# Kernel tuning notes

Measured on AMD Instinct MI355X. Metric: run time of the kernel, lower is better.

The kernel has to match this reference:

```python
import jax, jax.numpy as jnp
import numpy as np


def setup_inputs() -> dict:
    key = jax.random.key(0)
    k1, k2, k3, k4 = jax.random.split(key, 4)
    B, T, C, H = 32, 2048, 384, 64
    x = jax.random.normal(k1, (B, T, C), dtype=jnp.float32)
    # nn.Linear(C, H, bias=False): weight stored [H, C], applied as x @ W.T.
    # We store the transposed [C, H] form directly.
    s = 1.0 / np.sqrt(C)
    Wk = jax.random.normal(k2, (C, H), dtype=jnp.float32) * s
    Wq = jax.random.normal(k3, (C, H), dtype=jnp.float32) * s
    Wv = jax.random.normal(k4, (C, H), dtype=jnp.float32) * s
    return {"x": x, "Wk": Wk, "Wq": Wq, "Wv": Wv}


def reference(x, Wk, Wq, Wv):
    # x: [B, T, C]; Wk/Wq/Wv: [C, H]
    T = x.shape[1]
    H = Wk.shape[1]
    k = jnp.einsum('btc,ch->bth', x, Wk)
    q = jnp.einsum('btc,ch->bth', x, Wq)
    v = jnp.einsum('btc,ch->bth', x, Wv)
    scale = H ** (-0.5)
    scores = jnp.einsum('bth,bsh->bts', q, k) * scale  # [B, T, T]
    causal = jnp.tril(jnp.ones((T, T), dtype=bool))
    scores = jnp.where(causal, scores, -jnp.inf)
    attn = jax.nn.softmax(scores, axis=-1)
    # dropout is identity in eval mode
    out = jnp.einsum('bts,bsh->bth', attn, v)  # [B, T, H]
    return out
```

## Files before the change

kernel.cpp:

```cpp
#include <hip/hip_runtime.h>

typedef __bf16 bf16_8 __attribute__((ext_vector_type(8)));
typedef __bf16 bf16_4 __attribute__((ext_vector_type(4)));
typedef float  f32x4  __attribute__((ext_vector_type(4)));

#define NB 32
#define NT 2048
#define NC 384
#define NH 64

static __device__ __forceinline__ f32x4 mfma16(bf16_8 a, bf16_8 b, f32x4 c) {
  return __builtin_amdgcn_mfma_f32_16x16x32_bf16(a, b, c, 0, 0, 0);
}

__global__ void pack_w_kernel(const float* __restrict__ Wk, const float* __restrict__ Wq,
                              const float* __restrict__ Wv, __bf16* __restrict__ Wt) {
  int idx = blockIdx.x * 256 + threadIdx.x;
  if (idx >= 192 * NC) return;
  int n = idx / NC, k = idx % NC;
  int sel = n >> 6, h = n & 63;
  const float* W = (sel == 0) ? Wq : (sel == 1 ? Wk : Wv);
  float v = W[k * NH + h];
  if (sel == 0) v *= 0.125f * 1.44269504088896340736f;
  Wt[idx] = (__bf16)v;
}

__launch_bounds__(1024, 4)
__global__ void qkv_kernel(const float* __restrict__ x, const __bf16* __restrict__ Wt,
                           __bf16* __restrict__ Q, __bf16* __restrict__ K,
                           __bf16* __restrict__ Vt) {
  __shared__ __bf16 Wl[192 * 384];

  const int tid  = threadIdx.x;
  const int lane = tid & 63, wq = tid >> 6;
  const int quad = lane >> 4, l16 = lane & 15;
  const int rowblk = blockIdx.x * 256;
  const int rbase  = rowblk + wq * 16;
  const int row    = rbase + l16;

  #pragma unroll
  for (int i = 0; i < 9; ++i) {
    int g = tid + i * 1024;
    int r = g / 48, c = g - r * 48;
    int p = c ^ (r & 7);
    uint4 v = ((const uint4*)Wt)[g];
    *(uint4*)&Wl[(r * 48 + p) * 8] = v;
  }
  __syncthreads();

  f32x4 acc[12];
  #pragma unroll
  for (int n = 0; n < 12; ++n) acc[n] = f32x4{0.f, 0.f, 0.f, 0.f};

  const float* xrow = x + (size_t)row * NC;
  f32x4 x0 = *(const f32x4*)(xrow + quad * 8);
  f32x4 x1 = *(const f32x4*)(xrow + quad * 8 + 4);

  #pragma unroll
  for (int kc = 0; kc < 12; ++kc) {
    f32x4 nx0, nx1;
    if (kc < 11) {
      const float* xp = xrow + (kc + 1) * 32 + quad * 8;
      nx0 = *(const f32x4*)xp;
      nx1 = *(const f32x4*)(xp + 4);
    }
    bf16_8 a;
    a[0] = (__bf16)x0[0]; a[1] = (__bf16)x0[1]; a[2] = (__bf16)x0[2]; a[3] = (__bf16)x0[3];
    a[4] = (__bf16)x1[0]; a[5] = (__bf16)x1[1]; a[6] = (__bf16)x1[2]; a[7] = (__bf16)x1[3];
    const int pc = (kc * 4 + quad) ^ (l16 & 7);
    const int cbase = l16 * 48 + pc;
    #pragma unroll
    for (int n = 0; n < 12; ++n) {
      bf16_8 b = *(const bf16_8*)&Wl[(n * 16 * 48 + cbase) * 8];
      acc[n] = mfma16(a, b, acc[n]);
    }
    x0 = nx0; x1 = nx1;
  }

  __syncthreads();
  __bf16 (*Qs)[72]  = (__bf16(*)[72])Wl;
  __bf16 (*Ks2)[72] = (__bf16(*)[72])(Wl + 18432);
  __bf16 (*Vl)[264] = (__bf16(*)[264])(Wl + 36864);

  #pragma unroll
  for (int n = 0; n < 4; ++n)
    #pragma unroll
    for (int r = 0; r < 4; ++r) {
      int t = wq * 16 + quad * 4 + r;
      int h = n * 16 + l16;
      Qs[t][h]  = (__bf16)acc[n][r];
      Ks2[t][h] = (__bf16)acc[n + 4][r];
    }
  #pragma unroll
  for (int n = 8; n < 12; ++n) {
    int h = (n - 8) * 16 + l16;
    int t0 = wq * 16 + quad * 4;
    bf16_4 p;
    p[0] = (__bf16)acc[n][0]; p[1] = (__bf16)acc[n][1];
    p[2] = (__bf16)acc[n][2]; p[3] = (__bf16)acc[n][3];
    *(bf16_4*)&Vl[h][t0] = p;
  }
  __syncthreads();

  {
    int t = tid >> 2, h0 = (tid & 3) * 16;
    __bf16* qdst = Q + (size_t)(rowblk + t) * NH + h0;
    __bf16* kdst = K + (size_t)(rowblk + t) * NH + h0;
    const __bf16* qsrc = &Qs[t][h0];
    const __bf16* ksrc = &Ks2[t][h0];
    ((uint4*)qdst)[0] = ((const uint4*)qsrc)[0];
    ((uint4*)qdst)[1] = ((const uint4*)qsrc)[1];
    ((uint4*)kdst)[0] = ((const uint4*)ksrc)[0];
    ((uint4*)kdst)[1] = ((const uint4*)ksrc)[1];
  }
  {
    int h = tid >> 4, seg = tid & 15;
    int bb = rowblk >> 11, t0 = (rowblk & (NT - 1)) + seg * 16;
    const __bf16* src = &Vl[h][seg * 16];
    __bf16* dst = Vt + ((size_t)(bb * NH + h)) * NT + t0;
    ((uint4*)dst)[0] = ((const uint4*)src)[0];
    ((uint4*)dst)[1] = ((const uint4*)src)[1];
  }
}

__launch_bounds__(256)
__global__ void attn_kernel(const __bf16* __restrict__ Q, const __bf16* __restrict__ K,
                            const __bf16* __restrict__ Vt, float* __restrict__ out) {
  __shared__ __bf16 Ks[2][64][72];
  __shared__ __bf16 Vs[2][64][72];
  __shared__ __bf16 Ps[4][16][72];

  const int tid  = threadIdx.x;
  const int lane = tid & 63, wq = tid >> 6;
  const int quad = lane >> 4, l16 = lane & 15;
  const int b    = blockIdx.x >> 4;
  const int pair = blockIdx.x & 15;

  const float NEG_INF = -__builtin_inff();
  const float RTHR = 8.f;
  const int r = tid >> 2, seg = tid & 3;
  const __bf16* Kg = K  + (size_t)b * NT * NH;
  const __bf16* Vg = Vt + (size_t)b * NH * NT;

  for (int pass = 0; pass < 2; ++pass) {
    const int qt = pass ? pair : (31 - pair);
    const int q0 = qt * 64;
    const int nIter = qt + 1;

    const __bf16* qrow = Q + ((size_t)(b * NT + q0 + wq * 16 + l16)) * NH + quad * 8;
    bf16_8 qf0 = *(const bf16_8*)qrow;
    bf16_8 qf1 = *(const bf16_8*)(qrow + 32);

    f32x4 o[4];
    #pragma unroll
    for (int i = 0; i < 4; ++i) o[i] = f32x4{0.f, 0.f, 0.f, 0.f};
    float m_i = NEG_INF, l_i = 0.f;

    __syncthreads();

    {
      const uint4* sK = (const uint4*)(Kg + (size_t)r * NH + seg * 16);
      uint4 ka = sK[0], kb = sK[1];
      const uint4* sV = (const uint4*)(Vg + (size_t)r * NT + seg * 16);
      uint4 va = sV[0], vb = sV[1];
      *(uint4*)&Ks[0][r][seg * 16]     = ka;
      *(uint4*)&Ks[0][r][seg * 16 + 8] = kb;
      *(uint4*)&Vs[0][r][seg * 16]     = va;
      *(uint4*)&Vs[0][r][seg * 16 + 8] = vb;
    }

    for (int i = 0; i < nIter; ++i) {
      const int cur = i & 1;
      const bool more = (i + 1 < nIter);
      uint4 nka, nkb, nva, nvb;
      if (more) {
        const int s0n = (i + 1) * 64;
        const uint4* sK = (const uint4*)(Kg + (size_t)(s0n + r) * NH + seg * 16);
        nka = sK[0]; nkb = sK[1];
        const uint4* sV = (const uint4*)(Vg + (size_t)r * NT + s0n + seg * 16);
        nva = sV[0]; nvb = sV[1];
      }
      __syncthreads();

      f32x4 s[4];
      __builtin_amdgcn_s_setprio(1);
      #pragma unroll
      for (int st = 0; st < 4; ++st) {
        bf16_8 a0 = *(const bf16_8*)&Ks[cur][st * 16 + l16][quad * 8];
        bf16_8 a1 = *(const bf16_8*)&Ks[cur][st * 16 + l16][quad * 8 + 32];
        f32x4 accv = f32x4{0.f, 0.f, 0.f, 0.f};
        accv = mfma16(a0, qf0, accv);
        accv = mfma16(a1, qf1, accv);
        s[st] = accv;
      }
      __builtin_amdgcn_s_setprio(0);

      if (i == qt) {
        int qg = wq * 16 + l16;
        #pragma unroll
        for (int st = 0; st < 4; ++st)
          #pragma unroll
          for (int rr = 0; rr < 4; ++rr) {
            int sg = st * 16 + quad * 4 + rr;
            if (sg > qg) s[st][rr] = NEG_INF;
          }
      }

      float mx = NEG_INF;
      #pragma unroll
      for (int st = 0; st < 4; ++st)
        #pragma unroll
        for (int rr = 0; rr < 4; ++rr) mx = fmaxf(mx, s[st][rr]);
      mx = fmaxf(mx, __shfl_xor(mx, 16));
      mx = fmaxf(mx, __shfl_xor(mx, 32));

      float m_new = fmaxf(m_i, mx);
      if (__any(m_new - m_i > RTHR)) {
        float alpha = exp2f(m_i - m_new);
        f32x4 av;
        #pragma unroll
        for (int rr = 0; rr < 4; ++rr) av[rr] = __shfl(alpha, quad * 4 + rr);
        #pragma unroll
        for (int nt = 0; nt < 4; ++nt)
          #pragma unroll
          for (int rr = 0; rr < 4; ++rr) o[nt][rr] *= av[rr];
        l_i *= alpha;
        m_i = m_new;
      }

      float lsum = 0.f;
      #pragma unroll
      for (int st = 0; st < 4; ++st) {
        bf16_4 pk;
        #pragma unroll
        for (int rr = 0; rr < 4; ++rr) {
          float p = exp2f(s[st][rr] - m_i);
          lsum += p;
          pk[rr] = (__bf16)p;
        }
        *(bf16_4*)&Ps[wq][l16][st * 16 + quad * 4] = pk;
      }
      lsum += __shfl_xor(lsum, 16);
      lsum += __shfl_xor(lsum, 32);
      l_i += lsum;

      bf16_8 pa0 = *(const bf16_8*)&Ps[wq][l16][quad * 8];
      bf16_8 pa1 = *(const bf16_8*)&Ps[wq][l16][quad * 8 + 32];
      __builtin_amdgcn_s_setprio(1);
      #pragma unroll
      for (int nt = 0; nt < 4; ++nt) {
        bf16_8 b0 = *(const bf16_8*)&Vs[cur][nt * 16 + l16][quad * 8];
        bf16_8 b1 = *(const bf16_8*)&Vs[cur][nt * 16 + l16][quad * 8 + 32];
        o[nt] = mfma16(pa0, b0, o[nt]);
        o[nt] = mfma16(pa1, b1, o[nt]);
      }
      __builtin_amdgcn_s_setprio(0);

      if (more) {
        *(uint4*)&Ks[1 - cur][r][seg * 16]     = nka;
        *(uint4*)&Ks[1 - cur][r][seg * 16 + 8] = nkb;
        *(uint4*)&Vs[1 - cur][r][seg * 16]     = nva;
        *(uint4*)&Vs[1 - cur][r][seg * 16 + 8] = nvb;
      }
    }

    f32x4 lv;
    #pragma unroll
    for (int rr = 0; rr < 4; ++rr) lv[rr] = 1.f / __shfl(l_i, quad * 4 + rr);
    float* op = out + ((size_t)(b * NT + q0 + wq * 16 + quad * 4)) * NH + l16;
    #pragma unroll
    for (int nt = 0; nt < 4; ++nt)
      #pragma unroll
      for (int rr = 0; rr < 4; ++rr)
        op[(size_t)rr * NH + nt * 16] = o[nt][rr] * lv[rr];
  }
}

extern "C" void kernel_launch(void* const* d_in, const int* in_sizes, int n_in,
                              void* d_out, int out_size, void* d_ws, size_t ws_size,
                              hipStream_t stream) {
  const float* x  = (const float*)d_in[0];
  const float* Wk = (const float*)d_in[1];
  const float* Wq = (const float*)d_in[2];
  const float* Wv = (const float*)d_in[3];
  float* out = (float*)d_out;

  char* ws = (char*)d_ws;
  __bf16* Wt  = (__bf16*)ws;
  __bf16* Qb  = (__bf16*)(ws + 256 * 1024);
  __bf16* Kb  = Qb + (size_t)NB * NT * NH;
  __bf16* Vtb = Kb + (size_t)NB * NT * NH;

  pack_w_kernel<<<288, 256, 0, stream>>>(Wk, Wq, Wv, Wt);
  qkv_kernel<<<256, 1024, 0, stream>>>(x, Wt, Qb, Kb, Vtb);
  attn_kernel<<<NB * 16, 256, 0, stream>>>(Qb, Kb, Vtb, out);
}
```

Before: 210.9 us.

## Keep softmax probabilities in registers by permuting V's key layout in LDS

Removes the per-wave Ps shared-memory round trip: the exp'd scores are packed straight into the MFMA A-operand registers. Because the score accumulator layout does not match the A-operand k ordering, the V tile is written to LDS with a permuted key order so the PV product stays consistent. This drops an LDS write/read pair per iteration but replaces 16-byte V stores with scattered 8-byte stores, which can add bank conflicts.

```diff
diff --git a/kernel.cpp b/kernel.cpp
--- a/kernel.cpp
+++ b/kernel.cpp
@@ -128,7 +128,6 @@
                             const __bf16* __restrict__ Vt, float* __restrict__ out) {
   __shared__ __bf16 Ks[2][64][72];
   __shared__ __bf16 Vs[2][64][72];
-  __shared__ __bf16 Ps[4][16][72];
 
   const int tid  = threadIdx.x;
   const int lane = tid & 63, wq = tid >> 6;
@@ -141,6 +140,12 @@
   const int r = tid >> 2, seg = tid & 3;
   const __bf16* Kg = K  + (size_t)b * NT * NH;
   const __bf16* Vg = Vt + (size_t)b * NH * NT;
+
+  const int c0 = seg * 4;
+  const int kp0 = ((c0 & 8) << 2) + ((c0 & 3) << 3) + (((c0 >> 2) & 1) << 2);
+  const int kp1 = (((c0+1) & 8) << 2) + (((c0+1) & 3) << 3) + ((((c0+1) >> 2) & 1) << 2);
+  const int kp2 = (((c0+2) & 8) << 2) + (((c0+2) & 3) << 3) + ((((c0+2) >> 2) & 1) << 2);
+  const int kp3 = (((c0+3) & 8) << 2) + (((c0+3) & 3) << 3) + ((((c0+3) >> 2) & 1) << 2);
 
   for (int pass = 0; pass < 2; ++pass) {
     const int qt = pass ? pair : (31 - pair);
@@ -165,8 +170,10 @@
       uint4 va = sV[0], vb = sV[1];
       *(uint4*)&Ks[0][r][seg * 16]     = ka;
       *(uint4*)&Ks[0][r][seg * 16 + 8] = kb;
-      *(uint4*)&Vs[0][r][seg * 16]     = va;
-      *(uint4*)&Vs[0][r][seg * 16 + 8] = vb;
+      *(uint2*)&Vs[0][r][kp0] = make_uint2(va.x, va.y);
+      *(uint2*)&Vs[0][r][kp1] = make_uint2(va.z, va.w);
+      *(uint2*)&Vs[0][r][kp2] = make_uint2(vb.x, vb.y);
+      *(uint2*)&Vs[0][r][kp3] = make_uint2(vb.z, vb.w);
     }
 
     for (int i = 0; i < nIter; ++i) {
@@ -229,23 +236,21 @@
       }
 
       float lsum = 0.f;
-      #pragma unroll
-      for (int st = 0; st < 4; ++st) {
-        bf16_4 pk;
+      bf16_8 pa0, pa1;
+      #pragma unroll
+      for (int st = 0; st < 4; ++st)
         #pragma unroll
         for (int rr = 0; rr < 4; ++rr) {
           float p = exp2f(s[st][rr] - m_i);
           lsum += p;
-          pk[rr] = (__bf16)p;
+          __bf16 pb = (__bf16)p;
+          if (st < 2) pa0[st * 4 + rr] = pb;
+          else        pa1[(st - 2) * 4 + rr] = pb;
         }
-        *(bf16_4*)&Ps[wq][l16][st * 16 + quad * 4] = pk;
-      }
       lsum += __shfl_xor(lsum, 16);
       lsum += __shfl_xor(lsum, 32);
       l_i += lsum;
 
-      bf16_8 pa0 = *(const bf16_8*)&Ps[wq][l16][quad * 8];
-      bf16_8 pa1 = *(const bf16_8*)&Ps[wq][l16][quad * 8 + 32];
       __builtin_amdgcn_s_setprio(1);
       #pragma unroll
       for (int nt = 0; nt < 4; ++nt) {
@@ -259,8 +264,10 @@
       if (more) {
         *(uint4*)&Ks[1 - cur][r][seg * 16]     = nka;
         *(uint4*)&Ks[1 - cur][r][seg * 16 + 8] = nkb;
-        *(uint4*)&Vs[1 - cur][r][seg * 16]     = nva;
-        *(uint4*)&Vs[1 - cur][r][seg * 16 + 8] = nvb;
+        *(uint2*)&Vs[1 - cur][r][kp0] = make_uint2(nva.x, nva.y);
+        *(uint2*)&Vs[1 - cur][r][kp1] = make_uint2(nva.z, nva.w);
+        *(uint2*)&Vs[1 - cur][r][kp2] = make_uint2(nvb.x, nvb.y);
+        *(uint2*)&Vs[1 - cur][r][kp3] = make_uint2(nvb.z, nvb.w);
       }
     }
 
```

Measured after the change: 207.3 us. Within noise of the previous version (-1.7%).
